# Kernel optimization log

Measured on AMD Instinct MI355X. Metric: run time of the kernel, lower is better.

The kernel has to match this reference:

```python
import jax, jax.numpy as jnp
import numpy as np

N = 50000      # nodes
E = 400000     # edges (before self-loops)
D_IN = 128     # input node features
H1, C1 = 8, 64   # layer-1 heads / per-head channels (concat -> 512)
H2, C2 = 1, 16   # layer-2 heads / per-head channels (mean -> 16)
NEG_SLOPE = 0.2  # PyG GATConv default leaky-relu slope


def setup_inputs() -> dict:
    key = jax.random.key(0)
    ks = jax.random.split(key, 10)
    x = jax.random.normal(ks[0], (N, D_IN), jnp.float32)
    edge_index = jax.random.randint(ks[1], (2, E), 0, N, dtype=jnp.int32)
    s1 = D_IN ** -0.5
    s2 = (H1 * C1) ** -0.5
    return {
        "x": x,
        "edge_index": edge_index,
        "W1": jax.random.normal(ks[2], (D_IN, H1 * C1), jnp.float32) * s1,
        "a1_src": jax.random.normal(ks[3], (H1, C1), jnp.float32) * (C1 ** -0.5),
        "a1_dst": jax.random.normal(ks[4], (H1, C1), jnp.float32) * (C1 ** -0.5),
        "b1": jnp.zeros((H1 * C1,), jnp.float32),
        "W2": jax.random.normal(ks[5], (H1 * C1, H2 * C2), jnp.float32) * s2,
        "a2_src": jax.random.normal(ks[6], (H2, C2), jnp.float32) * (C2 ** -0.5),
        "a2_dst": jax.random.normal(ks[7], (H2, C2), jnp.float32) * (C2 ** -0.5),
        "b2": jnp.zeros((C2,), jnp.float32),
    }


def gat_layer(x, W, a_src, a_dst, bias, src, dst, H, C, concat):
    n = x.shape[0]
    h = (x @ W).reshape(n, H, C)                       # [N,H,C]
    # per-node attention halves (PyG: alpha = a_src . h_src + a_dst . h_dst)
    al_src = jnp.einsum('nhc,hc->nh', h, a_src)        # [N,H]
    al_dst = jnp.einsum('nhc,hc->nh', h, a_dst)
    logits = jax.nn.leaky_relu(al_src[src] + al_dst[dst], NEG_SLOPE)  # [E,H]
    # segment softmax over incoming edges of each destination node
    m = jax.ops.segment_max(logits, dst, num_segments=n)
    e = jnp.exp(logits - m[dst])
    denom = jax.ops.segment_sum(e, dst, num_segments=n)
    alpha = e / denom[dst]                             # [E,H]
    out = jax.ops.segment_sum(alpha[:, :, None] * h[src], dst, num_segments=n)  # [N,H,C]
    out = out.reshape(n, H * C) if concat else out.mean(axis=1)
    return out + bias


def reference(x, edge_index, W1, a1_src, a1_dst, b1, W2, a2_src, a2_dst, b2):
    n = x.shape[0]
    # PyG GATConv adds self-loops by default (applied in each layer)
    loops = jnp.arange(n, dtype=edge_index.dtype)
    src = jnp.concatenate([edge_index[0], loops])
    dst = jnp.concatenate([edge_index[1], loops])
    h1 = gat_layer(x, W1, a1_src, a1_dst, b1, src, dst, H1, C1, True)   # [N,512]
    h1 = jax.nn.elu(h1)
    return gat_layer(h1, W2, a2_src, a2_dst, b2, src, dst, H2, C2, False)  # [N,16]
```

## Files before the change

kernel.cpp:

```cpp
#include <hip/hip_runtime.h>
#include <math.h>

#define N_NODES 50000
#define N_EDGES 400000
#define N_TOT   450000
#define NEG 0.2f
#define CAP 64

typedef __attribute__((ext_vector_type(8))) short bf16x8;
typedef __attribute__((ext_vector_type(8))) unsigned short u16x8;
typedef __attribute__((ext_vector_type(4))) float f32x4;

__device__ __forceinline__ float lrelu(float x) { return x > 0.f ? x : NEG * x; }

__device__ __forceinline__ unsigned short f2bf(float f) {
    unsigned u = __float_as_uint(f);
    unsigned r = u + 0x7FFFu + ((u >> 16) & 1u);
    return (unsigned short)(r >> 16);
}
__device__ __forceinline__ float bf2f(unsigned short h) {
    return __uint_as_float(((unsigned)h) << 16);
}

__global__ void k_init(const float* __restrict__ W1, unsigned short* W1hiT,
                       const float* __restrict__ W2, unsigned short* W2hiT,
                       const float* __restrict__ a1s, const float* __restrict__ a1d,
                       unsigned short* W1aThi, unsigned short* W1aTlo,
                       int* cursor) {
    int i = blockIdx.x * 256 + threadIdx.x;
    if (i < 128 * 512) {
        int col = i & 511, k = i >> 9;
        W1hiT[col * 128 + k] = f2bf(W1[k * 512 + col]);
    } else if (i < 128 * 512 + 512 * 16) {
        int j = i - 128 * 512;
        int col = j & 15, k = j >> 4;
        W2hiT[col * 512 + k] = f2bf(W2[k * 16 + col]);
    } else if (i < 128 * 512 + 512 * 16 + 128 * 16) {
        int j = i - (128 * 512 + 512 * 16);
        int c16 = j & 15, k = j >> 4;
        int hd = c16 & 7;
        const float* av = (c16 < 8) ? a1s : a1d;
        float acc = 0.f;
#pragma unroll 8
        for (int c = 0; c < 64; c++)
            acc = fmaf(W1[k * 512 + hd * 64 + c], av[hd * 64 + c], acc);
        unsigned short h = f2bf(acc);
        W1aThi[c16 * 128 + k] = h;
        W1aTlo[c16 * 128 + k] = f2bf(acc - bf2f(h));
    } else {
        int j = i - (128 * 512 + 512 * 16 + 128 * 16);
        if (j < N_NODES) cursor[j] = 0;
    }
}

#define SCAT 256
__global__ __launch_bounds__(256) void k_sg1(const int* __restrict__ ei,
                                             int* __restrict__ cursor,
                                             int* __restrict__ colsrc,
                                             const float* __restrict__ x,
                                             const unsigned short* __restrict__ W1hiT,
                                             const unsigned short* __restrict__ W1aThi,
                                             const unsigned short* __restrict__ W1aTlo,
                                             unsigned short* __restrict__ h1b,
                                             float* __restrict__ al1s,
                                             float* __restrict__ al1d) {
    __shared__ unsigned short xs_hi[64 * 136];
    if (blockIdx.x < SCAT) {
        int gtid = blockIdx.x * 256 + threadIdx.x;
        for (int i = gtid; i < N_TOT; i += SCAT * 256) {
            int src, dst;
            if (i < N_EDGES) { src = ei[i]; dst = ei[N_EDGES + i]; }
            else             { src = dst = i - N_EDGES; }
            int pos = atomicAdd(&cursor[dst], 1);
            if (pos < CAP) colsrc[dst * CAP + pos] = src;
        }
        return;
    }
    const int t = threadIdx.x;
    const int rb = (blockIdx.x - SCAT) * 64;

#pragma unroll
    for (int i = 0; i < 8; i++) {
        int idx = t + 256 * i;
        int r = idx >> 5;
        int k = (idx & 31) * 4;
        int gr = rb + r;
        float4 v = make_float4(0.f, 0.f, 0.f, 0.f);
        if (gr < N_NODES) v = *reinterpret_cast<const float4*>(&x[gr * 128 + k]);
        ushort4 hi;
        hi.x = f2bf(v.x); hi.y = f2bf(v.y); hi.z = f2bf(v.z); hi.w = f2bf(v.w);
        *reinterpret_cast<ushort4*>(&xs_hi[r * 136 + k]) = hi;
    }
    __syncthreads();

    const int lane = t & 63;
    const int w = t >> 6;
    const int kbase = (lane >> 4) * 8;
    const int colloc = (w << 4) + (lane & 15);

#pragma unroll
    for (int pr = 0; pr < 4; pr++) {
        bf16x8 bhi[2][4];
#pragma unroll
        for (int si = 0; si < 2; si++) {
            int col = (pr * 2 + si) * 64 + colloc;
#pragma unroll
            for (int kc = 0; kc < 4; kc++)
                bhi[si][kc] = *reinterpret_cast<const bf16x8*>(&W1hiT[col * 128 + kc * 32 + kbase]);
        }
#pragma unroll
        for (int mt = 0; mt < 4; mt++) {
            const int arow = mt * 16 + (lane & 15);
            bf16x8 ah[4];
#pragma unroll
            for (int kc = 0; kc < 4; kc++)
                ah[kc] = *reinterpret_cast<const bf16x8*>(&xs_hi[arow * 136 + kc * 32 + kbase]);
#pragma unroll
            for (int si = 0; si < 2; si++) {
                f32x4 acc = {0.f, 0.f, 0.f, 0.f};
#pragma unroll
                for (int kc = 0; kc < 4; kc++)
                    acc = __builtin_amdgcn_mfma_f32_16x16x32_bf16(ah[kc], bhi[si][kc], acc, 0, 0, 0);
                const int col = (pr * 2 + si) * 64 + colloc;
                const int r0 = rb + mt * 16 + (lane >> 4) * 4;
#pragma unroll
                for (int r = 0; r < 4; r++) {
                    int row = r0 + r;
                    if (row < N_NODES) h1b[row * 512 + col] = f2bf(acc[r]);
                }
            }
        }
    }

    {
        const int c16 = lane & 15;
        bf16x8 bh[4], bl[4];
#pragma unroll
        for (int kc = 0; kc < 4; kc++) {
            bh[kc] = *reinterpret_cast<const bf16x8*>(&W1aThi[c16 * 128 + kc * 32 + kbase]);
            bl[kc] = *reinterpret_cast<const bf16x8*>(&W1aTlo[c16 * 128 + kc * 32 + kbase]);
        }
        const int arow = (w << 4) + (lane & 15);
        f32x4 acc = {0.f, 0.f, 0.f, 0.f};
#pragma unroll
        for (int kc = 0; kc < 4; kc++) {
            bf16x8 ah = *reinterpret_cast<const bf16x8*>(&xs_hi[arow * 136 + kc * 32 + kbase]);
            acc = __builtin_amdgcn_mfma_f32_16x16x32_bf16(ah, bh[kc], acc, 0, 0, 0);
            acc = __builtin_amdgcn_mfma_f32_16x16x32_bf16(ah, bl[kc], acc, 0, 0, 0);
        }
        const int r0 = rb + (w << 4) + (lane >> 4) * 4;
#pragma unroll
        for (int r = 0; r < 4; r++) {
            int row = r0 + r;
            if (row < N_NODES) {
                if (c16 < 8) al1s[row * 8 + c16] = acc[r];
                else         al1d[row * 8 + (c16 - 8)] = acc[r];
            }
        }
    }
}

__global__ __launch_bounds__(256) void k_agg1(const int* __restrict__ cursor,
                                              const int* __restrict__ colsrc,
                                              const float* __restrict__ al1s,
                                              const float* __restrict__ al1d,
                                              const unsigned short* __restrict__ h1b,
                                              const float* __restrict__ b1,
                                              const unsigned short* __restrict__ W2hiT,
                                              const float* __restrict__ a2s,
                                              const float* __restrict__ a2d,
                                              unsigned short* __restrict__ h2b,
                                              float* __restrict__ al2s,
                                              float* __restrict__ al2d) {
    __shared__ float pw[4][8 * 66];
    __shared__ int se[4][64];
    __shared__ __align__(16) unsigned short vs[4 * 520];
    const int wid  = threadIdx.x >> 6;
    const int lane = threadIdx.x & 63;
    const int n0 = blockIdx.x * 4;
    const int n  = n0 + wid;
    const int cnt = min(cursor[n], CAP);
    const int eb = n * CAP;
    const int h  = lane >> 3;
    const int c8 = lane << 3;
    float* mypw = pw[wid];
    const int* mysrc = se[wid];

    const float4 d0 = *reinterpret_cast<const float4*>(&al1d[n * 8]);
    const float4 d1 = *reinterpret_cast<const float4*>(&al1d[n * 8 + 4]);

    int s0 = 0;
    float p[8];
    if (lane < cnt) {
        s0 = colsrc[eb + lane];
        const float4 u0 = *reinterpret_cast<const float4*>(&al1s[s0 * 8]);
        const float4 u1 = *reinterpret_cast<const float4*>(&al1s[s0 * 8 + 4]);
        p[0] = __expf(fminf(lrelu(u0.x + d0.x), 60.f));
        p[1] = __expf(fminf(lrelu(u0.y + d0.y), 60.f));
        p[2] = __expf(fminf(lrelu(u0.z + d0.z), 60.f));
        p[3] = __expf(fminf(lrelu(u0.w + d0.w), 60.f));
        p[4] = __expf(fminf(lrelu(u1.x + d1.x), 60.f));
        p[5] = __expf(fminf(lrelu(u1.y + d1.y), 60.f));
        p[6] = __expf(fminf(lrelu(u1.z + d1.z), 60.f));
        p[7] = __expf(fminf(lrelu(u1.w + d1.w), 60.f));
    } else {
#pragma unroll
        for (int hh = 0; hh < 8; hh++) p[hh] = 0.f;
    }
    se[wid][lane] = s0;
#pragma unroll
    for (int hh = 0; hh < 8; hh++) mypw[hh * 66 + lane] = p[hh];

    float acc[8] = {0.f, 0.f, 0.f, 0.f, 0.f, 0.f, 0.f, 0.f};
    float sm = 0.f;
    const int pwh = h * 66;

    int j = 0;
    for (; j + 7 < cnt; j += 8) {
        int4 sa = *reinterpret_cast<const int4*>(&mysrc[j]);
        int4 sb = *reinterpret_cast<const int4*>(&mysrc[j + 4]);
        u16x8 e0 = *reinterpret_cast<const u16x8*>(&h1b[sa.x * 512 + c8]);
        u16x8 e1 = *reinterpret_cast<const u16x8*>(&h1b[sa.y * 512 + c8]);
        u16x8 e2 = *reinterpret_cast<const u16x8*>(&h1b[sa.z * 512 + c8]);
        u16x8 e3 = *reinterpret_cast<const u16x8*>(&h1b[sa.w * 512 + c8]);
        u16x8 e4 = *reinterpret_cast<const u16x8*>(&h1b[sb.x * 512 + c8]);
        u16x8 e5 = *reinterpret_cast<const u16x8*>(&h1b[sb.y * 512 + c8]);
        u16x8 e6 = *reinterpret_cast<const u16x8*>(&h1b[sb.z * 512 + c8]);
        u16x8 e7 = *reinterpret_cast<const u16x8*>(&h1b[sb.w * 512 + c8]);
        float w0 = mypw[pwh + j + 0], w1 = mypw[pwh + j + 1];
        float w2 = mypw[pwh + j + 2], w3 = mypw[pwh + j + 3];
        float w4 = mypw[pwh + j + 4], w5 = mypw[pwh + j + 5];
        float w6 = mypw[pwh + j + 6], w7 = mypw[pwh + j + 7];
        sm += ((w0 + w1) + (w2 + w3)) + ((w4 + w5) + (w6 + w7));
#pragma unroll
        for (int c = 0; c < 8; c++) {
            float t = fmaf(w0, bf2f(e0[c]), acc[c]);
            t = fmaf(w1, bf2f(e1[c]), t);
            t = fmaf(w2, bf2f(e2[c]), t);
            t = fmaf(w3, bf2f(e3[c]), t);
            t = fmaf(w4, bf2f(e4[c]), t);
            t = fmaf(w5, bf2f(e5[c]), t);
            t = fmaf(w6, bf2f(e6[c]), t);
            acc[c] = fmaf(w7, bf2f(e7[c]), t);
        }
    }
    for (; j < cnt; j += 4) {
        int4 sa = *reinterpret_cast<const int4*>(&mysrc[j]);
        u16x8 e0 = *reinterpret_cast<const u16x8*>(&h1b[sa.x * 512 + c8]);
        u16x8 e1 = *reinterpret_cast<const u16x8*>(&h1b[sa.y * 512 + c8]);
        u16x8 e2 = *reinterpret_cast<const u16x8*>(&h1b[sa.z * 512 + c8]);
        u16x8 e3 = *reinterpret_cast<const u16x8*>(&h1b[sa.w * 512 + c8]);
        float w0 = mypw[pwh + j + 0], w1 = mypw[pwh + j + 1];
        float w2 = mypw[pwh + j + 2], w3 = mypw[pwh + j + 3];
        sm += (w0 + w1) + (w2 + w3);
#pragma unroll
        for (int c = 0; c < 8; c++) {
            float t = fmaf(w0, bf2f(e0[c]), acc[c]);
            t = fmaf(w1, bf2f(e1[c]), t);
            t = fmaf(w2, bf2f(e2[c]), t);
            acc[c] = fmaf(w3, bf2f(e3[c]), t);
        }
    }

    const float inv = 1.f / sm;
    const float4 ba = *reinterpret_cast<const float4*>(&b1[c8]);
    const float4 bb = *reinterpret_cast<const float4*>(&b1[c8 + 4]);
    float v[8];
    v[0] = acc[0] * inv + ba.x; v[1] = acc[1] * inv + ba.y;
    v[2] = acc[2] * inv + ba.z; v[3] = acc[3] * inv + ba.w;
    v[4] = acc[4] * inv + bb.x; v[5] = acc[5] * inv + bb.y;
    v[6] = acc[6] * inv + bb.z; v[7] = acc[7] * inv + bb.w;
#pragma unroll
    for (int k = 0; k < 8; k++)
        v[k] = v[k] > 0.f ? v[k] : __expf(v[k]) - 1.f;
    u16x8 o;
#pragma unroll
    for (int k = 0; k < 8; k++) o[k] = f2bf(v[k]);
    *reinterpret_cast<u16x8*>(&vs[wid * 520 + c8]) = o;

    __syncthreads();

    if (wid == 0) {
        const int col   = lane & 15;
        const int kbase = (lane >> 4) << 3;
        const int rowm  = lane & 3;
        f32x4 a2 = {0.f, 0.f, 0.f, 0.f};
#pragma unroll 4
        for (int kc = 0; kc < 16; kc++) {
            bf16x8 bh = *reinterpret_cast<const bf16x8*>(&W2hiT[col * 512 + kc * 32 + kbase]);
            bf16x8 ah = *reinterpret_cast<const bf16x8*>(&vs[rowm * 520 + kc * 32 + kbase]);
            a2 = __builtin_amdgcn_mfma_f32_16x16x32_bf16(ah, bh, a2, 0, 0, 0);
        }
        if (lane < 16) {
            const float as_c = a2s[col];
            const float ad_c = a2d[col];
#pragma unroll
            for (int r = 0; r < 4; r++) {
                float ps = a2[r] * as_c;
                float pd = a2[r] * ad_c;
                ps += __shfl_xor(ps, 1, 64); pd += __shfl_xor(pd, 1, 64);
                ps += __shfl_xor(ps, 2, 64); pd += __shfl_xor(pd, 2, 64);
                ps += __shfl_xor(ps, 4, 64); pd += __shfl_xor(pd, 4, 64);
                ps += __shfl_xor(ps, 8, 64); pd += __shfl_xor(pd, 8, 64);
                h2b[(n0 + r) * 16 + col] = f2bf(a2[r]);
                if (lane == 0) { al2s[n0 + r] = ps; al2d[n0 + r] = pd; }
            }
        }
    }
}

__global__ __launch_bounds__(256) void k_agg2(const int* __restrict__ cursor,
                                              const int* __restrict__ colsrc,
                                              const float* __restrict__ al2s,
                                              const float* __restrict__ al2d,
                                              const unsigned short* __restrict__ h2b,
                                              const float* __restrict__ b2,
                                              float* __restrict__ out) {
    int wv = threadIdx.x >> 6, lane = threadIdx.x & 63;
    int n = blockIdx.x * 4 + wv;
    if (n >= N_NODES) return;
    int cnt = min(cursor[n], CAP);
    const int eb = n * CAP;
    float ald = al2d[n];
    int q = lane >> 2;
    int c4 = (lane & 3) << 2;
    float a0 = 0.f, a1 = 0.f, a2 = 0.f, a3 = 0.f, smL = 0.f;
    for (int e = q; e < cnt; e += 16) {
        int s = colsrc[eb + e];
        float w = __expf(fminf(lrelu(al2s[s] + ald), 60.f));
        ushort4 v = *reinterpret_cast<const ushort4*>(&h2b[s * 16 + c4]);
        smL += w;
        a0 = fmaf(w, bf2f(v.x), a0);
        a1 = fmaf(w, bf2f(v.y), a1);
        a2 = fmaf(w, bf2f(v.z), a2);
        a3 = fmaf(w, bf2f(v.w), a3);
    }
#pragma unroll
    for (int off = 4; off < 64; off <<= 1) {
        a0 += __shfl_xor(a0, off, 64);
        a1 += __shfl_xor(a1, off, 64);
        a2 += __shfl_xor(a2, off, 64);
        a3 += __shfl_xor(a3, off, 64);
        smL += __shfl_xor(smL, off, 64);
    }
    if (q == 0) {
        float inv = 1.f / smL;
        const float4 bb = *reinterpret_cast<const float4*>(&b2[c4]);
        float4 r;
        r.x = a0 * inv + bb.x;
        r.y = a1 * inv + bb.y;
        r.z = a2 * inv + bb.z;
        r.w = a3 * inv + bb.w;
        *reinterpret_cast<float4*>(&out[n * 16 + c4]) = r;
    }
}

extern "C" void kernel_launch(void* const* d_in, const int* in_sizes, int n_in,
                              void* d_out, int out_size, void* d_ws, size_t ws_size,
                              hipStream_t stream) {
    const float* x   = (const float*)d_in[0];
    const int*   ei  = (const int*)d_in[1];
    const float* W1  = (const float*)d_in[2];
    const float* a1s = (const float*)d_in[3];
    const float* a1d = (const float*)d_in[4];
    const float* b1  = (const float*)d_in[5];
    const float* W2  = (const float*)d_in[6];
    const float* a2s = (const float*)d_in[7];
    const float* a2d = (const float*)d_in[8];
    const float* b2  = (const float*)d_in[9];
    float* out = (float*)d_out;

    char* ws = (char*)d_ws;
    unsigned short* h1b = (unsigned short*)(ws + 0);
    unsigned short* h2b = (unsigned short*)(ws + 102400000);
    float* al1s = (float*)(ws + 105600000);
    float* al1d = (float*)(ws + 107200000);
    float* al2s = (float*)(ws + 108800000);
    float* al2d = (float*)(ws + 109000000);
    int* cursor = (int*)(ws + 109200000);
    int* colsrc = (int*)(ws + 109400000);
    unsigned short* W1hiT  = (unsigned short*)(ws + 122200000);
    unsigned short* W2hiT  = (unsigned short*)(ws + 122336000);
    unsigned short* W1aThi = (unsigned short*)(ws + 122352384);
    unsigned short* W1aTlo = (unsigned short*)(ws + 122356480);

    k_init<<<492, 256, 0, stream>>>(W1, W1hiT, W2, W2hiT, a1s, a1d, W1aThi, W1aTlo, cursor);

    k_sg1<<<SCAT + (N_NODES + 63) / 64, 256, 0, stream>>>(ei, cursor, colsrc, x,
                                                          W1hiT, W1aThi, W1aTlo,
                                                          h1b, al1s, al1d);

    k_agg1<<<(N_NODES + 3) / 4, 256, 0, stream>>>(cursor, colsrc, al1s, al1d, h1b, b1,
                                                  W2hiT, a2s, a2d, h2b, al2s, al2d);

    k_agg2<<<(N_NODES + 3) / 4, 256, 0, stream>>>(cursor, colsrc, al2s, al2d, h2b, b2, out);
}
```

Measured before the change: 223.9 us.

## Pre-seed self-loops in init, widen scatter grid, shuffle source indices in aggregation

Self-loop entries are now written in k_init by setting each cursor to 1 and colsrc[n*CAP] = n, so the scatter loop handles only real edges. The scatter part of k_sg1 is launched with more blocks. In k_agg1, source indices are broadcast with wavefront shuffles instead of going through shared memory, and the gather loop is reworked from 8-wide to 4-wide unrolling with a one-at-a-time tail. This removes the self-loop atomics and an LDS staging step, at the cost of fewer loads in flight per iteration and a different floating-point summation order.

```diff
diff --git a/kernel.cpp b/kernel.cpp
--- a/kernel.cpp
+++ b/kernel.cpp
@@ -26,7 +26,7 @@
                        const float* __restrict__ W2, unsigned short* W2hiT,
                        const float* __restrict__ a1s, const float* __restrict__ a1d,
                        unsigned short* W1aThi, unsigned short* W1aTlo,
-                       int* cursor) {
+                       int* cursor, int* colsrc) {
     int i = blockIdx.x * 256 + threadIdx.x;
     if (i < 128 * 512) {
         int col = i & 511, k = i >> 9;
@@ -49,11 +49,14 @@
         W1aTlo[c16 * 128 + k] = f2bf(acc - bf2f(h));
     } else {
         int j = i - (128 * 512 + 512 * 16 + 128 * 16);
-        if (j < N_NODES) cursor[j] = 0;
-    }
-}
-
-#define SCAT 256
+        if (j < N_NODES) {
+            cursor[j] = 1;
+            colsrc[j * CAP] = j;
+        }
+    }
+}
+
+#define SCAT 1024
 __global__ __launch_bounds__(256) void k_sg1(const int* __restrict__ ei,
                                              int* __restrict__ cursor,
                                              int* __restrict__ colsrc,
@@ -67,10 +70,9 @@
     __shared__ unsigned short xs_hi[64 * 136];
     if (blockIdx.x < SCAT) {
         int gtid = blockIdx.x * 256 + threadIdx.x;
-        for (int i = gtid; i < N_TOT; i += SCAT * 256) {
-            int src, dst;
-            if (i < N_EDGES) { src = ei[i]; dst = ei[N_EDGES + i]; }
-            else             { src = dst = i - N_EDGES; }
+        for (int i = gtid; i < N_EDGES; i += SCAT * 256) {
+            int src = ei[i];
+            int dst = ei[N_EDGES + i];
             int pos = atomicAdd(&cursor[dst], 1);
             if (pos < CAP) colsrc[dst * CAP + pos] = src;
         }
@@ -173,7 +175,6 @@
                                               float* __restrict__ al2s,
                                               float* __restrict__ al2d) {
     __shared__ float pw[4][8 * 66];
-    __shared__ int se[4][64];
     __shared__ __align__(16) unsigned short vs[4 * 520];
     const int wid  = threadIdx.x >> 6;
     const int lane = threadIdx.x & 63;
@@ -184,7 +185,6 @@
     const int h  = lane >> 3;
     const int c8 = lane << 3;
     float* mypw = pw[wid];
-    const int* mysrc = se[wid];
 
     const float4 d0 = *reinterpret_cast<const float4*>(&al1d[n * 8]);
     const float4 d1 = *reinterpret_cast<const float4*>(&al1d[n * 8 + 4]);
@@ -207,7 +207,6 @@
 #pragma unroll
         for (int hh = 0; hh < 8; hh++) p[hh] = 0.f;
     }
-    se[wid][lane] = s0;
 #pragma unroll
     for (int hh = 0; hh < 8; hh++) mypw[hh * 66 + lane] = p[hh];
 
@@ -216,50 +215,31 @@
     const int pwh = h * 66;
 
     int j = 0;
-    for (; j + 7 < cnt; j += 8) {
-        int4 sa = *reinterpret_cast<const int4*>(&mysrc[j]);
-        int4 sb = *reinterpret_cast<const int4*>(&mysrc[j + 4]);
-        u16x8 e0 = *reinterpret_cast<const u16x8*>(&h1b[sa.x * 512 + c8]);
-        u16x8 e1 = *reinterpret_cast<const u16x8*>(&h1b[sa.y * 512 + c8]);
-        u16x8 e2 = *reinterpret_cast<const u16x8*>(&h1b[sa.z * 512 + c8]);
-        u16x8 e3 = *reinterpret_cast<const u16x8*>(&h1b[sa.w * 512 + c8]);
-        u16x8 e4 = *reinterpret_cast<const u16x8*>(&h1b[sb.x * 512 + c8]);
-        u16x8 e5 = *reinterpret_cast<const u16x8*>(&h1b[sb.y * 512 + c8]);
-        u16x8 e6 = *reinterpret_cast<const u16x8*>(&h1b[sb.z * 512 + c8]);
-        u16x8 e7 = *reinterpret_cast<const u16x8*>(&h1b[sb.w * 512 + c8]);
-        float w0 = mypw[pwh + j + 0], w1 = mypw[pwh + j + 1];
-        float w2 = mypw[pwh + j + 2], w3 = mypw[pwh + j + 3];
-        float w4 = mypw[pwh + j + 4], w5 = mypw[pwh + j + 5];
-        float w6 = mypw[pwh + j + 6], w7 = mypw[pwh + j + 7];
-        sm += ((w0 + w1) + (w2 + w3)) + ((w4 + w5) + (w6 + w7));
-#pragma unroll
-        for (int c = 0; c < 8; c++) {
-            float t = fmaf(w0, bf2f(e0[c]), acc[c]);
-            t = fmaf(w1, bf2f(e1[c]), t);
-            t = fmaf(w2, bf2f(e2[c]), t);
-            t = fmaf(w3, bf2f(e3[c]), t);
-            t = fmaf(w4, bf2f(e4[c]), t);
-            t = fmaf(w5, bf2f(e5[c]), t);
-            t = fmaf(w6, bf2f(e6[c]), t);
-            acc[c] = fmaf(w7, bf2f(e7[c]), t);
-        }
-    }
-    for (; j < cnt; j += 4) {
-        int4 sa = *reinterpret_cast<const int4*>(&mysrc[j]);
-        u16x8 e0 = *reinterpret_cast<const u16x8*>(&h1b[sa.x * 512 + c8]);
-        u16x8 e1 = *reinterpret_cast<const u16x8*>(&h1b[sa.y * 512 + c8]);
-        u16x8 e2 = *reinterpret_cast<const u16x8*>(&h1b[sa.z * 512 + c8]);
-        u16x8 e3 = *reinterpret_cast<const u16x8*>(&h1b[sa.w * 512 + c8]);
-        float w0 = mypw[pwh + j + 0], w1 = mypw[pwh + j + 1];
-        float w2 = mypw[pwh + j + 2], w3 = mypw[pwh + j + 3];
-        sm += (w0 + w1) + (w2 + w3);
-#pragma unroll
-        for (int c = 0; c < 8; c++) {
-            float t = fmaf(w0, bf2f(e0[c]), acc[c]);
-            t = fmaf(w1, bf2f(e1[c]), t);
-            t = fmaf(w2, bf2f(e2[c]), t);
-            acc[c] = fmaf(w3, bf2f(e3[c]), t);
-        }
+    for (; j + 3 < cnt; j += 4) {
+        int s[4]; float w[4]; u16x8 vv[4];
+#pragma unroll
+        for (int k = 0; k < 4; k++) {
+            s[k] = __shfl(s0, j + k, 64);
+            w[k] = mypw[pwh + j + k];
+        }
+#pragma unroll
+        for (int k = 0; k < 4; k++)
+            vv[k] = *reinterpret_cast<const u16x8*>(&h1b[s[k] * 512 + c8]);
+#pragma unroll
+        for (int k = 0; k < 4; k++) {
+            sm += w[k];
+#pragma unroll
+            for (int c = 0; c < 8; c++)
+                acc[c] = fmaf(w[k], bf2f(vv[k][c]), acc[c]);
+        }
+    }
+    for (; j < cnt; ++j) {
+        int s = __shfl(s0, j, 64);
+        u16x8 v = *reinterpret_cast<const u16x8*>(&h1b[s * 512 + c8]);
+        float w = mypw[pwh + j];
+        sm += w;
+#pragma unroll
+        for (int c = 0; c < 8; c++) acc[c] = fmaf(w, bf2f(v[c]), acc[c]);
     }
 
     const float inv = 1.f / sm;
@@ -384,7 +364,8 @@
     unsigned short* W1aThi = (unsigned short*)(ws + 122352384);
     unsigned short* W1aTlo = (unsigned short*)(ws + 122356480);
 
-    k_init<<<492, 256, 0, stream>>>(W1, W1hiT, W2, W2hiT, a1s, a1d, W1aThi, W1aTlo, cursor);
+    k_init<<<492, 256, 0, stream>>>(W1, W1hiT, W2, W2hiT, a1s, a1d, W1aThi, W1aTlo,
+                                    cursor, colsrc);
 
     k_sg1<<<SCAT + (N_NODES + 63) / 64, 256, 0, stream>>>(ei, cursor, colsrc, x,
                                                           W1hiT, W1aThi, W1aTlo,
```

Result: slower. 228.8 us (+2.2%).
